# Kernel tuning notes

Measured on AMD Instinct MI355X. Metric: run time of the kernel, lower is better.

Reference implementation:

```python
import jax, jax.numpy as jnp
import numpy as np

P = 11  # corr_size (patch size of spatial_correlation_sample)
LEVELS = [(512, 64), (1024, 32), (512, 16), (256, 8), (256, 4), (256, 2)]  # (C, H) per pyramid level
B = 8


def _corr(f1, f2, p):
    # spatial_correlation_sample(kernel_size=1, patch_size=p, stride=1, padding=0, dilation_patch=1)
    # out[b, i*p+j, y, x] = sum_c f1[b,c,y,x] * f2[b,c,y+i-p//2, x+j-p//2] (zero padded)
    b, c, h, w = f1.shape
    r = p // 2
    f2p = jnp.pad(f2, ((0, 0), (0, 0), (r, r), (r, r)))
    shifts = jnp.stack(jnp.meshgrid(jnp.arange(p), jnp.arange(p), indexing='ij'), axis=-1).reshape(-1, 2)
    def body(carry, sh):
        sl = jax.lax.dynamic_slice(f2p, (0, 0, sh[0], sh[1]), (b, c, h, w))
        return carry, jnp.sum(f1 * sl, axis=1)  # (b, h, w)
    _, out = jax.lax.scan(body, None, shifts)  # (p*p, b, h, w)
    return jnp.transpose(out, (1, 0, 2, 3))  # (b, p*p, h, w)


def _cell(feat, feat_pre, h_pre, c_pre, W, bias, p):
    corr = _corr(feat, feat_pre, p)
    corr = jnp.where(corr > 0, corr, 0.01 * corr)  # LeakyReLU(0.01)
    corr = corr / jnp.max(corr)                    # max-normalize
    inp = jnp.concatenate([corr, h_pre], axis=1)   # (b, 2*p*p, h, w)
    conv = jax.lax.conv_general_dilated(
        inp, W, window_strides=(1, 1), padding=[(1, 1), (1, 1)],
        dimension_numbers=('NCHW', 'OIHW', 'NCHW')) + bias[None, :, None, None]
    cc_i, cc_f, cc_o, cc_g = jnp.split(conv, 4, axis=1)
    i = jax.nn.sigmoid(cc_i)
    f = jax.nn.sigmoid(cc_f)
    o = jax.nn.sigmoid(cc_o)
    g = jnp.tanh(cc_g)
    c_next = f * c_pre + i * g
    h_next = o * jnp.tanh(c_next)
    return h_next, c_next


def setup_inputs():
    key = jax.random.key(0)
    inp = {}
    for i, (C, H) in enumerate(LEVELS):
        ks = jax.random.split(jax.random.fold_in(key, i), 5)
        inp[f"x{i}"] = jax.random.normal(ks[0], (B, C, H, H), jnp.float32)
        inp[f"xp{i}"] = jax.random.normal(ks[1], (B, C, H, H), jnp.float32)
        inp[f"h{i}"] = jax.random.normal(ks[2], (B, P * P, H, H), jnp.float32)
        inp[f"c{i}"] = jax.random.normal(ks[3], (B, P * P, H, H), jnp.float32)
        inp[f"W{i}"] = jax.random.normal(ks[4], (4 * P * P, 2 * P * P, 3, 3), jnp.float32) * 0.02
        # bias: forget-gate slice initialized to 1 (as in init_weights)
        inp[f"bconv{i}"] = jnp.zeros((4 * P * P,), jnp.float32).at[P * P:2 * P * P].set(1.0)
    return inp


def reference(x0, x1, x2, x3, x4, x5, xp0, xp1, xp2, xp3, xp4, xp5,
              h0, h1, h2, h3, h4, h5, c0, c1, c2, c3, c4, c5,
              W0, W1, W2, W3, W4, W5, bconv0, bconv1, bconv2, bconv3, bconv4, bconv5):
    xs = [x0, x1, x2, x3, x4, x5]
    xps = [xp0, xp1, xp2, xp3, xp4, xp5]
    hs = [h0, h1, h2, h3, h4, h5]
    cs = [c0, c1, c2, c3, c4, c5]
    Ws = [W0, W1, W2, W3, W4, W5]
    bs = [bconv0, bconv1, bconv2, bconv3, bconv4, bconv5]
    outs = []
    for feat, fp, hp, cp, W, bias in zip(xs, xps, hs, cs, Ws, bs):
        hn, cn = _cell(feat, fp, hp, cp, W, bias, P)
        outs.extend([hn, cn])
    return tuple(outs)
```

## Files before the change

kernel.cpp:

```cpp
#include <hip/hip_runtime.h>
#include <hip/hip_bf16.h>
#include <cstdint>
#include <cstddef>

#define PD 11
#define PP 121
#define NB 8

typedef _Float16 f16x8 __attribute__((ext_vector_type(8)));
typedef float    f32x4 __attribute__((ext_vector_type(4)));

#define GLOAD16(SRC, DST) __builtin_amdgcn_global_load_lds( \
    (const __attribute__((address_space(1))) void*)(SRC),   \
    (__attribute__((address_space(3))) void*)(DST), 16, 0, 0)

struct TinyArgs {
    const float* x[3]; const float* xp[3]; const float* h[3];
    const float* c[3]; const float* w[3]; const float* bi[3];
    float* oh[3]; float* oc[3];
};

struct BigArgs {
    const float *x1, *xp1, *x2, *xp2;
    _Float16 *xT1, *xpT1, *xT2, *xpT2;
    _Float16 *inT0, *inT1, *inT2;
    const float *h0, *h1, *h2;
    const float *W0, *W1, *W2;
    _Float16 *ap0, *ap1, *ap2;
    unsigned* slots;
    const _Float16* zg;
};

struct ConvArgs {
    const _Float16 *inT0, *inT1, *inT2, *tinyInT;
    const float *c0, *c1, *c2;
    const _Float16 *ap0, *ap1, *ap2;
    const _Float16 *apT0, *apT1, *apT2;
    const float *bi0, *bi1, *bi2;
    float *oh0, *oc0, *oh1, *oc1, *oh2, *oc2;
    const _Float16* zg;
    TinyArgs ta;
};

__global__ void init_kernel(unsigned* __restrict__ slots, float* __restrict__ zg) {
    int t = threadIdx.x;
    if (t < 8) slots[t] = 0x007FFFFFu;
    for (int i = t; i < 1024; i += 256) zg[i] = 0.f;
}

__device__ __forceinline__ float decode_max(const unsigned* slot) {
    unsigned mu = *slot;
    return (mu & 0x80000000u) ? __uint_as_float(mu ^ 0x80000000u) : __uint_as_float(~mu);
}

template<int C, int H, int TPX>
__device__ void tpose_body(const float* __restrict__ in, _Float16* __restrict__ out,
                           int bx, int by, int tid, float (*s)[36])
{
    constexpr int W = H;
    const int b  = by / H, y = by % H;
    constexpr int NXT = W / TPX;
    const int x0 = (bx % NXT) * TPX;
    const int cc = (bx / NXT) * 64;

    constexpr int NF4 = 64 * TPX / 4;
    for (int f = tid; f < NF4; f += 256) {
        int r  = f / (TPX / 4);
        int xq = f % (TPX / 4);
        int col = (xq * 4) ^ (((r >> 3) & 7) * 4);
        *(float4*)&s[r][col] =
            *(const float4*)&in[((size_t)(b * C + cc + r) * H + y) * W + x0 + xq * 4];
    }
    __syncthreads();
    constexpr int NWT = TPX * 8;
    for (int t = tid; t < NWT; t += 256) {
        int pix = t >> 3, ck = t & 7;
        union { _Float16 h[8]; f16x8 v; } d;
#pragma unroll
        for (int j = 0; j < 8; ++j)
            d.h[j] = (_Float16)s[ck * 8 + j][pix ^ (ck * 4)];
        *(f16x8*)&out[((size_t)(b * H + y) * W + x0 + pix) * C + cc + ck * 8] = d.v;
    }
}

template<int C, int H, int TPX>
__global__ __launch_bounds__(256) void tpose_kernel(
    const float* __restrict__ xin, const float* __restrict__ xpin,
    _Float16* __restrict__ xT, _Float16* __restrict__ xpT)
{
    __shared__ float s[64][36];
    tpose_body<C, H, TPX>(blockIdx.z ? xpin : xin, blockIdx.z ? xpT : xT,
                          blockIdx.x, blockIdx.y, threadIdx.x, s);
}

template<int C, int H, int TSY, int TSX>
constexpr int corr_lds() {
    constexpr int HY = TSY + 10, HX = TSX + 10;
    constexpr int MZ = HY * HX;
    constexpr int MT = (MZ + 15) / 16;
    constexpr int MTP = MT * 16;
    constexpr int NPX = TSY * TSX;
    constexpr int BUF = (MTP + NPX) * 64;
    constexpr int ST2 = NPX + 8;
    constexpr int ST_B = MTP * ST2 * 2;
    return (2 * BUF > ST_B) ? 2 * BUF : ST_B;
}

template<int C, int H, int TSY, int TSX>
__device__ void corr_body(
    const _Float16* __restrict__ xT, const _Float16* __restrict__ xpT,
    const _Float16* __restrict__ zg,
    _Float16* __restrict__ inT, unsigned* __restrict__ slot,
    int bxt, int b, char* __restrict__ smem, float* __restrict__ sred)
{
    constexpr int W  = H;
    constexpr int HY = TSY + 10, HX = TSX + 10;
    constexpr int MZ = HY * HX;
    constexpr int MT = (MZ + 15) / 16;
    constexpr int MTP = MT * 16;
    constexpr int MFRAG = (MT + 7) / 8;
    constexpr int NPX = TSY * TSX;
    constexpr int NT  = NPX / 16;
    constexpr int KC  = C / 32;
    constexpr int ABYTES = MTP * 64;
    constexpr int BUF    = ABYTES + NPX * 64;
    constexpr int NLOAD  = BUF / 1024;
    constexpr int ST2    = NPX + 8;

    const int tid  = threadIdx.x;
    constexpr int TXT = W / TSX;
    const int y0 = (bxt / TXT) * TSY;
    const int x0 = (bxt % TXT) * TSX;
    const int w = tid >> 6, lane = tid & 63;
    const int lcol = lane & 15, lkg = lane >> 4;

    auto STAGE = [&](int bufsel, int kc) {
        char* dstb = smem + bufsel * BUF;
        int c = lane & 3;
        for (int it = w; it < NLOAD; it += 8) {
            const void* src;
            if (it < MTP / 16) {
                int z = it * 16 + (lane >> 2);
                int zy = y0 + z / HX - 5, zx = x0 + z % HX - 5;
                if (z < MZ && zy >= 0 && zy < H && zx >= 0 && zx < W)
                    src = xpT + ((size_t)(b * H + zy) * W + zx) * C + kc * 32 + ((c ^ (z >> 2)) & 3) * 8;
                else
                    src = zg + lane * 8;
            } else {
                int p = (it - MTP / 16) * 16 + (lane >> 2);
                int gy = y0 + p / TSX, gx = x0 + p % TSX;
                src = xT + ((size_t)(b * H + gy) * W + gx) * C + kc * 32 + ((c ^ (p >> 2)) & 3) * 8;
            }
            GLOAD16(src, dstb + it * 1024);
        }
    };

    f32x4 acc[MFRAG][NT];
#pragma unroll
    for (int i = 0; i < MFRAG; ++i)
#pragma unroll
        for (int nt = 0; nt < NT; ++nt)
            acc[i][nt] = (f32x4){0.f, 0.f, 0.f, 0.f};

    STAGE(0, 0);
    __syncthreads();
#pragma unroll 1
    for (int kc = 0; kc < KC; ++kc) {
        if (kc + 1 < KC) STAGE((kc + 1) & 1, kc + 1);
        const char* bb = smem + (kc & 1) * BUF;
        f16x8 bF[NT];
#pragma unroll
        for (int nt = 0; nt < NT; ++nt) {
            int p = nt * 16 + lcol;
            bF[nt] = *(const f16x8*)(bb + ABYTES + p * 64 + (((lkg ^ (p >> 2)) & 3) << 4));
        }
#pragma unroll
        for (int i = 0; i < MFRAG; ++i) {
            int mt = w + i * 8;
            if (mt < MT) {
                int z = mt * 16 + lcol;
                f16x8 aF = *(const f16x8*)(bb + z * 64 + (((lkg ^ (z >> 2)) & 3) << 4));
#pragma unroll
                for (int nt = 0; nt < NT; ++nt)
                    acc[i][nt] = __builtin_amdgcn_mfma_f32_16x16x32_f16(aF, bF[nt], acc[i][nt], 0, 0, 0);
            }
        }
        __syncthreads();
    }

    _Float16* sT = (_Float16*)smem;
#pragma unroll
    for (int i = 0; i < MFRAG; ++i) {
        int mt = w + i * 8;
        if (mt >= MT) continue;
        int z0 = mt * 16 + lkg * 4;
#pragma unroll
        for (int nt = 0; nt < NT; ++nt) {
            int p = nt * 16 + lcol;
#pragma unroll
            for (int r = 0; r < 4; ++r)
                sT[(z0 + r) * ST2 + p] = (_Float16)acc[i][nt][r];
        }
    }
    __syncthreads();

    float lmax = -3.4e38f;
    if (tid < NPX * 8) {
        int p  = tid >> 3;
        int qg = tid & 7;
        int py = p / TSX, px = p % TSX;
        size_t pix = (size_t)(b * H + y0 + py) * W + (x0 + px);
        unsigned* dst = (unsigned*)(inT + pix * 256) + qg * 8;
#pragma unroll
        for (int j2 = 0; j2 < 8; ++j2) {
            int q0 = qg * 16 + j2 * 2, q1 = q0 + 1;
            int qc0 = q0 < PP ? q0 : PP - 1;
            int qc1 = q1 < PP ? q1 : PP - 1;
            float v0 = (float)sT[((py + qc0 / PD) * HX + (px + qc0 % PD)) * ST2 + p];
            float v1 = (float)sT[((py + qc1 / PD) * HX + (px + qc1 % PD)) * ST2 + p];
            v0 = v0 > 0.f ? v0 : 0.01f * v0;
            v1 = v1 > 0.f ? v1 : 0.01f * v1;
            if (q0 < PP) lmax = fmaxf(lmax, v0);
            if (q1 < PP) lmax = fmaxf(lmax, v1);
            union { _Float16 h[2]; unsigned u; } pk;
            pk.h[0] = (_Float16)v0; pk.h[1] = (_Float16)v1;
            dst[j2] = pk.u;
        }
    }
    for (int off = 32; off; off >>= 1) lmax = fmaxf(lmax, __shfl_down(lmax, off));
    if (lane == 0) sred[w] = lmax;
    __syncthreads();
    if (tid == 0) {
        float m = sred[0];
        for (int i = 1; i < 8; ++i) m = fmaxf(m, sred[i]);
        unsigned eb = __float_as_uint(m);
        eb = (eb & 0x80000000u) ? ~eb : (eb | 0x80000000u);
        atomicMax(slot, eb);
    }
}

template<int C, int H, int TSY, int TSX>
__global__ __launch_bounds__(512, 2) void corr_mfma_kernel(
    const _Float16* __restrict__ xT, const _Float16* __restrict__ xpT,
    const _Float16* __restrict__ zg,
    _Float16* __restrict__ inT, unsigned* __restrict__ slot)
{
    __shared__ char smem[corr_lds<C, H, TSY, TSX>()];
    __shared__ float sred[8];
    corr_body<C, H, TSY, TSX>(xT, xpT, zg, inT, slot, blockIdx.x, blockIdx.y, smem, sred);
}

__device__ __forceinline__ void pack2_body(
    const float* __restrict__ Wsrc, _Float16* __restrict__ Apack,
    float inv, int mt, int ks, int tid, float* __restrict__ sW)
{
    const int icmax9 = (242 - ks * 32) * 9;
    for (int f = tid; f < 16 * 288; f += 256) {
        int r = f / 288, i = f - r * 288;
        int m = mt * 16 + r;
        float v = 0.f;
        if (m < 484 && i < icmax9) {
            int q = m >> 2, g = m & 3;
            v = Wsrc[((size_t)(g * PP + q) * 242 + ks * 32) * 9 + i];
        }
        sW[r * 292 + i] = v;
    }
    __syncthreads();
    const int o = tid * 2;
    const int l = o >> 3, e0 = o & 7;
    const int r = l & 15;
    const int klbase = (l >> 4) * 8;
    const int ic0 = ks * 32 + klbase + e0;
#pragma unroll 1
    for (int k9 = 0; k9 < 9; ++k9) {
        float v0 = sW[r * 292 + (klbase + e0) * 9 + k9];
        float v1 = sW[r * 292 + (klbase + e0 + 1) * 9 + k9];
        if (ic0 < PP)     v0 *= inv;
        if (ic0 + 1 < PP) v1 *= inv;
        union { _Float16 h[2]; unsigned u; } pk;
        pk.h[0] = (_Float16)v0; pk.h[1] = (_Float16)v1;
        *(unsigned*)((char*)Apack + (size_t)((k9 * 8 + ks) * 32 + mt) * 1024 + o * 2) = pk.u;
    }
}

template<int H>
__device__ void post_body(
    _Float16* __restrict__ inT, const float* __restrict__ hpre,
    const float* __restrict__ Wsrc, _Float16* __restrict__ Apack,
    const unsigned* __restrict__ slot, int bx, int tid, float* __restrict__ sW)
{
    if (bx < 256) {
        float inv = 1.0f / decode_max(slot);
        pack2_body(Wsrc, Apack, inv, bx >> 3, bx & 7, tid, sW);
        return;
    }
    constexpr int HW = H * H;
    constexpr int NP = NB * HW;
    int idx = (bx - 256) * 256 + tid;
    if (idx >= NP * 17) return;
    int c = 15 + idx / NP;
    int pix = idx % NP;
    int b = pix / HW, p2 = pix % HW;
    _Float16* base = inT + (size_t)pix * 256 + c * 8;
    union { _Float16 h[8]; uint4 u; } d;
    if (c == 15) {
        d.u = *(const uint4*)base;
#pragma unroll
        for (int j = 1; j < 8; ++j)
            d.h[j] = (_Float16)hpre[((size_t)b * PP + (j - 1)) * HW + p2];
    } else if (c <= 29) {
#pragma unroll
        for (int j = 0; j < 8; ++j)
            d.h[j] = (_Float16)hpre[((size_t)b * PP + (c * 8 + j - 121)) * HW + p2];
    } else if (c == 30) {
        d.h[0] = (_Float16)hpre[((size_t)b * PP + 119) * HW + p2];
        d.h[1] = (_Float16)hpre[((size_t)b * PP + 120) * HW + p2];
#pragma unroll
        for (int j = 2; j < 8; ++j) d.h[j] = (_Float16)0.f;
    } else {
#pragma unroll
        for (int j = 0; j < 8; ++j) d.h[j] = (_Float16)0.f;
    }
    *(uint4*)base = d.u;
}

template<int H>
__global__ __launch_bounds__(256) void post_kernel(
    _Float16* __restrict__ inT, const float* __restrict__ hpre,
    const float* __restrict__ Wsrc, _Float16* __restrict__ Apack,
    const unsigned* __restrict__ slot)
{
    __shared__ float sW[16 * 292];
    post_body<H>(inT, hpre, Wsrc, Apack, slot, blockIdx.x, threadIdx.x, sW);
}

template<int H>
__device__ void corr_small512_body(const float* __restrict__ x, const float* __restrict__ xp,
    _Float16* __restrict__ inT, unsigned* __restrict__ slot, int b, int bx,
    float* __restrict__ sred)
{
    constexpr int PX  = H * H;
    constexpr int TOT = PX * PP;
    const int tid = threadIdx.x;
    const int o = bx * 512 + tid;
    float v = -3.4e38f;
    if (o < TOT) {
        int p = o / PP;
        int q = o - p * PP;
        int y = p / H, xx = p % H;
        int sy = y + q / PD - 5, sx = xx + q % PD - 5;
        float acc = 0.f;
        if (sy >= 0 && sy < H && sx >= 0 && sx < H) {
            const float* xb  = x  + (size_t)b * 256 * PX + p;
            const float* xpb = xp + (size_t)b * 256 * PX + sy * H + sx;
#pragma unroll 8
            for (int c = 0; c < 256; ++c)
                acc = fmaf(xb[c * PX], xpb[c * PX], acc);
        }
        float lv = acc > 0.f ? acc : 0.01f * acc;
        inT[((size_t)b * PX + p) * 256 + q] = (_Float16)lv;
        v = lv;
    }
    for (int off = 32; off; off >>= 1) v = fmaxf(v, __shfl_down(v, off));
    if ((tid & 63) == 0) sred[tid >> 6] = v;
    __syncthreads();
    if (tid == 0) {
        float m = sred[0];
        for (int i = 1; i < 8; ++i) m = fmaxf(m, sred[i]);
        unsigned eb = __float_as_uint(m);
        eb = (eb & 0x80000000u) ? ~eb : (eb | 0x80000000u);
        atomicMax(slot, eb);
    }
}

template<int H>
__device__ void hfill_body(_Float16* __restrict__ inT, const float* __restrict__ hpre,
                           int b, int bx)
{
    constexpr int HW = H * H;
    int idx = bx * 256 + threadIdx.x;
    if (idx >= HW * 17) return;
    int c = 15 + idx / HW;
    int p2 = idx % HW;
    _Float16* base = inT + ((size_t)b * HW + p2) * 256 + c * 8;
    union { _Float16 h[8]; uint4 u; } d;
    if (c == 15) {
        d.u = *(const uint4*)base;
#pragma unroll
        for (int j = 1; j < 8; ++j)
            d.h[j] = (_Float16)hpre[((size_t)b * PP + (j - 1)) * HW + p2];
    } else if (c <= 29) {
#pragma unroll
        for (int j = 0; j < 8; ++j)
            d.h[j] = (_Float16)hpre[((size_t)b * PP + (c * 8 + j - 121)) * HW + p2];
    } else if (c == 30) {
        d.h[0] = (_Float16)hpre[((size_t)b * PP + 119) * HW + p2];
        d.h[1] = (_Float16)hpre[((size_t)b * PP + 120) * HW + p2];
#pragma unroll
        for (int j = 2; j < 8; ++j) d.h[j] = (_Float16)0.f;
    } else {
#pragma unroll
        for (int j = 0; j < 8; ++j) d.h[j] = (_Float16)0.f;
    }
    *(uint4*)base = d.u;
}

__global__ __launch_bounds__(256) void mixA_kernel(BigArgs ba, _Float16* __restrict__ inT0)
{
    __shared__ float sW[16 * 292];
    const int i = blockIdx.x, tid = threadIdx.x;
    if (i < 2432) {
        post_body<64>(inT0, ba.h0, ba.W0, ba.ap0, ba.slots + 0, i, tid, sW);
    } else if (i < 2432 + 8192) {
        int j = i - 2432;
        int z = j >> 12, r = j & 4095;
        tpose_body<1024, 32, 32>(z ? ba.xp1 : ba.x1, z ? ba.xpT1 : ba.xT1,
                                 r & 15, r >> 4, tid, (float(*)[36])sW);
    } else {
        int j = i - (2432 + 8192);
        int z = j >> 10, r = j & 1023;
        tpose_body<512, 16, 16>(z ? ba.xp2 : ba.x2, z ? ba.xpT2 : ba.xT2,
                                r & 7, r >> 3, tid, (float(*)[36])sW);
    }
}

__global__ __launch_bounds__(512, 2) void mixB_kernel(BigArgs ba, TinyArgs ta,
                                                      _Float16* __restrict__ tinyInT)
{
    __shared__ char smem[36864];
    __shared__ float sred[8];
    const int i = blockIdx.x;
    if (i < 256) {
        corr_body<1024, 32, 4, 8>(ba.xT1, ba.xpT1, ba.zg, ba.inT1, ba.slots + 1,
                                  i & 31, i >> 5, smem, sred);
    } else if (i < 384) {
        int j = i - 256;
        corr_body<512, 16, 4, 4>(ba.xT2, ba.xpT2, ba.zg, ba.inT2, ba.slots + 2,
                                 j & 15, j >> 4, smem, sred);
    } else if (i < 512) {
        int j = i - 384;
        corr_small512_body<8>(ta.x[0], ta.xp[0], tinyInT, ba.slots + 3,
                              j >> 4, j & 15, sred);
    } else if (i < 544) {
        int j = i - 512;
        corr_small512_body<4>(ta.x[1], ta.xp[1], tinyInT + 131072, ba.slots + 4,
                              j >> 2, j & 3, sred);
    } else {
        int j = i - 544;
        corr_small512_body<2>(ta.x[2], ta.xp[2], tinyInT + 163840, ba.slots + 5,
                              j, 0, sred);
    }
}

__global__ __launch_bounds__(256) void mixC_kernel(BigArgs ba, TinyArgs ta,
    _Float16* __restrict__ tinyInT,
    _Float16* __restrict__ apT0, _Float16* __restrict__ apT1, _Float16* __restrict__ apT2)
{
    __shared__ float sW[16 * 292];
    const int i = blockIdx.x, tid = threadIdx.x;
    if (i < 800) {
        post_body<32>(ba.inT1, ba.h1, ba.W1, ba.ap1, ba.slots + 1, i, tid, sW);
    } else if (i < 1192) {
        post_body<16>(ba.inT2, ba.h2, ba.W2, ba.ap2, ba.slots + 2, i - 800, tid, sW);
    } else if (i < 1960) {
        int j = i - 1192;
        int z = j >> 8, bx = j & 255;
        _Float16* Ap = (z == 0) ? apT0 : (z == 1 ? apT1 : apT2);
        float inv = 1.0f / decode_max(ba.slots + 3 + z);
        pack2_body(ta.w[z], Ap, inv, bx >> 3, bx & 7, tid, sW);
    } else {
        int j = i - 1960;
        if (j < 40)      hfill_body<8>(tinyInT,          ta.h[0], j / 5, j % 5);
        else if (j < 56) { int k = j - 40; hfill_body<4>(tinyInT + 131072, ta.h[1], k / 2, k % 2); }
        else             hfill_body<2>(tinyInT + 163840, ta.h[2], j - 56, 0);
    }
}

template<int H, int TR, int MSPLIT>
__device__ void conv_mfma3_body(
    const _Float16* __restrict__ inT, const float* __restrict__ cpre,
    const _Float16* __restrict__ Apack, const float* __restrict__ bias,
    const _Float16* __restrict__ zg,
    float* __restrict__ outh, float* __restrict__ outc,
    int tile, int b, int mblk, char* __restrict__ sB)
{
    constexpr int W = H;
    constexpr int TC = 16, SR = TC + 2;
    constexpr int NPOS = (TR + 2) * SR;
    constexpr int MT_BLK = 32 / MSPLIT;
    constexpr int AF = 4 / MSPLIT;
    constexpr int TILES_X = W / TC;

    const int tid  = threadIdx.x;
    const int ty0  = (tile / TILES_X) * TR;
    const int tx0  = (tile % TILES_X) * TC;
    const int w = tid >> 6, lane = tid & 63;
    const int lcol = lane & 15, kg = lane >> 4;

    for (int it = w; it < NPOS / 2; it += 8) {
        int r  = it * 2 + (lane >> 5);
        int c  = lane & 31;
        int iy = r / SR, ix = r % SR;
        int gy = ty0 + iy - 1, gx = tx0 + ix - 1;
        const void* src;
        if (gy >= 0 && gy < H && gx >= 0 && gx < W)
            src = inT + ((size_t)(b * H + gy) * W + gx) * 256 + (c ^ (ix & 7)) * 8;
        else
            src = zg + lane * 8;
        GLOAD16(src, sB + it * 1024);
    }
    __syncthreads();

    const int mtg0 = mblk * MT_BLK + w * AF;

    f32x4 acc[AF * TR];
#pragma unroll
    for (int a = 0; a < AF; ++a) {
        int q = (mtg0 + a) * 4 + kg;
        f32x4 bv;
#pragma unroll
        for (int r = 0; r < 4; ++r) bv[r] = (q < PP) ? bias[r * PP + q] : 0.f;
#pragma unroll
        for (int j = 0; j < TR; ++j) acc[a * TR + j] = bv;
    }

    const f16x8* apL = (const f16x8*)Apack + (size_t)mtg0 * 64 + lane;

    auto COMPUTE = [&](const f16x8* af, int s) {
        int k9 = s >> 3, ks = s & 7;
        int ky = k9 / 3, kx = k9 - ky * 3;
        int ix = lcol + kx;
        int xsw = (ix & 7) << 4;
        int cb  = kg * 16 + ks * 64;
        __builtin_amdgcn_s_setprio(1);
#pragma unroll
        for (int j = 0; j < TR; ++j) {
            int addr = ((((j + ky) * SR + ix) * 512) + cb) ^ xsw;
            f16x8 bf = *(const f16x8*)(sB + addr);
#pragma unroll
            for (int a = 0; a < AF; ++a)
                acc[a * TR + j] = __builtin_amdgcn_mfma_f32_16x16x32_f16(af[a], bf, acc[a * TR + j], 0, 0, 0);
        }
        __builtin_amdgcn_s_setprio(0);
    };

    f16x8 afA[AF], afB[AF];
#pragma unroll
    for (int a = 0; a < AF; ++a) afA[a] = apL[a * 64];
#pragma unroll 1
    for (int s2 = 0; s2 < 36; ++s2) {
        const f16x8* apB = apL + (size_t)(s2 * 2 + 1) * 2048;
#pragma unroll
        for (int a = 0; a < AF; ++a) afB[a] = apB[a * 64];
        COMPUTE(afA, s2 * 2);
        if (s2 < 35) {
            const f16x8* apA = apL + (size_t)(s2 * 2 + 2) * 2048;
#pragma unroll
            for (int a = 0; a < AF; ++a) afA[a] = apA[a * 64];
        }
        COMPUTE(afB, s2 * 2 + 1);
    }

#pragma unroll
    for (int a = 0; a < AF; ++a) {
        int q = (mtg0 + a) * 4 + kg;
        if (q >= PP) continue;
#pragma unroll
        for (int j = 0; j < TR; ++j) {
            int y = ty0 + j, x = tx0 + lcol;
            if (y >= H) continue;
            float ai = acc[a * TR + j][0];
            float af_ = acc[a * TR + j][1];
            float ao = acc[a * TR + j][2];
            float ag = acc[a * TR + j][3];
            float ig = 1.f / (1.f + expf(-ai));
            float fg = 1.f / (1.f + expf(-af_));
            float og = 1.f / (1.f + expf(-ao));
            float gg = tanhf(ag);
            size_t oidx = (((size_t)b * PP + q) * H + y) * W + x;
            float cp = cpre[oidx];
            float cn = fg * cp + ig * gg;
            outh[oidx] = og * tanhf(cn);
            outc[oidx] = cn;
        }
    }
}

template<int H>
__device__ void conv_tiny_body(const _Float16* __restrict__ inT,
    const float* __restrict__ cpre, const _Float16* __restrict__ Apack,
    const float* __restrict__ bias, float* __restrict__ outh,
    float* __restrict__ outc, int b, int mblk, char* __restrict__ sB)
{
    constexpr int NPX = H * H;
    constexpr int NT  = (NPX + 15) / 16;
    constexpr int SR  = H + 2;
    constexpr int NPOS = SR * SR;
    const int tid = threadIdx.x;

    constexpr int CHUNKS = NPOS * 32;
    for (int flat = tid; flat < CHUNKS; flat += 512) {
        int cg  = flat & 31;
        int pos = flat >> 5;
        int iy = pos / SR, ix = pos % SR;
        int gy = iy - 1, gx = ix - 1;
        f16x8 v = {0, 0, 0, 0, 0, 0, 0, 0};
        if (gy >= 0 && gy < H && gx >= 0 && gx < H)
            v = *(const f16x8*)(inT + ((size_t)(b * H + gy) * H + gx) * 256 + cg * 8);
        int dst = (pos * 512 + cg * 16) ^ ((ix & 7) << 4);
        *(f16x8*)(sB + dst) = v;
    }
    __syncthreads();

    const int w = tid >> 6, lane = tid & 63;
    const int lcol = lane & 15, kg = lane >> 4;
    const int mt = mblk * 8 + w;
    const int q  = mt * 4 + kg;

    f32x4 acc[NT];
    f32x4 bv;
#pragma unroll
    for (int r = 0; r < 4; ++r) bv[r] = (q < PP) ? bias[r * PP + q] : 0.f;
#pragma unroll
    for (int nt = 0; nt < NT; ++nt) acc[nt] = bv;

#pragma unroll 1
    for (int k9 = 0; k9 < 9; ++k9) {
        const int ky = k9 / 3, kx = k9 % 3;
        int basev[NT], xswv[NT];
#pragma unroll
        for (int nt = 0; nt < NT; ++nt) {
            int p = nt * 16 + lcol;
            int pc = (NPX < 16 && p >= NPX) ? 0 : p;
            int py = pc / H, px = pc % H;
            int iy = py + ky, ix = px + kx;
            basev[nt] = (iy * SR + ix) * 512 + kg * 16;
            xswv[nt]  = (ix & 7) << 4;
        }
        const f16x8* apb = (const f16x8*)Apack + ((size_t)(k9 * 8) * 32 + mt) * 64 + lane;
#pragma unroll 1
        for (int ks = 0; ks < 8; ++ks) {
            f16x8 bf[NT];
#pragma unroll
            for (int nt = 0; nt < NT; ++nt) {
                bf[nt] = *(const f16x8*)(sB + ((basev[nt] + ks * 64) ^ xswv[nt]));
                if (NPX < 16 && nt * 16 + lcol >= NPX) bf[nt] = (f16x8){};
            }
            f16x8 af = apb[(size_t)ks * 32 * 64];
#pragma unroll
            for (int nt = 0; nt < NT; ++nt)
                acc[nt] = __builtin_amdgcn_mfma_f32_16x16x32_f16(af, bf[nt], acc[nt], 0, 0, 0);
        }
    }

    if (q < PP) {
#pragma unroll
        for (int nt = 0; nt < NT; ++nt) {
            int p = nt * 16 + lcol;
            if (NPX < 16 && p >= NPX) continue;
            int py = p / H, px = p % H;
            float ai = acc[nt][0];
            float af_ = acc[nt][1];
            float ao = acc[nt][2];
            float ag = acc[nt][3];
            float ig = 1.f / (1.f + expf(-ai));
            float fg = 1.f / (1.f + expf(-af_));
            float og = 1.f / (1.f + expf(-ao));
            float gg = tanhf(ag);
            size_t oidx = (((size_t)b * PP + q) * H + py) * H + px;
            float cp = cpre[oidx];
            float cn = fg * cp + ig * gg;
            outh[oidx] = og * tanhf(cn);
            outc[oidx] = cn;
        }
    }
}

__global__ __launch_bounds__(512, 4) void conv_combo_kernel(ConvArgs ca)
{
    __shared__ char sB[108 * 512];
    const int bx = blockIdx.x;
    if (bx < 512) {
        conv_mfma3_body<64, 4, 1>(ca.inT0, ca.c0, ca.ap0, ca.bi0, ca.zg,
                                  ca.oh0, ca.oc0, bx & 63, bx >> 6, 0, sB);
    } else if (bx < 768) {
        int i = bx - 512;
        conv_mfma3_body<32, 4, 2>(ca.inT1, ca.c1, ca.ap1, ca.bi1, ca.zg,
                                  ca.oh1, ca.oc1, i & 15, (i >> 4) & 7, i >> 7, sB);
    } else if (bx < 896) {
        int i = bx - 768;
        conv_mfma3_body<16, 4, 4>(ca.inT2, ca.c2, ca.ap2, ca.bi2, ca.zg,
                                  ca.oh2, ca.oc2, i & 3, (i >> 2) & 7, i >> 5, sB);
    } else {
        int j = bx - 896;
        int z = j >> 5, r = j & 31;
        int b = r >> 2, mblk = r & 3;
        if      (z == 0) conv_tiny_body<8>(ca.tinyInT,          ca.ta.c[0], ca.apT0, ca.ta.bi[0], ca.ta.oh[0], ca.ta.oc[0], b, mblk, sB);
        else if (z == 1) conv_tiny_body<4>(ca.tinyInT + 131072, ca.ta.c[1], ca.apT1, ca.ta.bi[1], ca.ta.oh[1], ca.ta.oc[1], b, mblk, sB);
        else             conv_tiny_body<2>(ca.tinyInT + 163840, ca.ta.c[2], ca.apT2, ca.ta.bi[2], ca.ta.oh[2], ca.ta.oc[2], b, mblk, sB);
    }
}

extern "C" void kernel_launch(void* const* d_in, const int* in_sizes, int n_in,
                              void* d_out, int out_size, void* d_ws, size_t ws_size,
                              hipStream_t stream) {
    (void)in_sizes; (void)n_in; (void)out_size; (void)ws_size;
    static const int HH[6] = {64, 32, 16, 8, 4, 2};

    char* W = (char*)d_ws;
    unsigned* maxslots = (unsigned*)W;
    _Float16* Apack0 = (_Float16*)(W + 256);
    _Float16* inT0   = (_Float16*)(W + 2359808);
    char* XB = W + 19137024;
    char* PB = W + 52691456;
    _Float16* xT0  = (_Float16*)XB;
    _Float16* xpT0 = (_Float16*)PB;
    _Float16* zg   = (_Float16*)(W + 86245888);

    BigArgs ba;
    ba.x1  = (const float*)d_in[6];  ba.xp1 = (const float*)d_in[7];
    ba.x2  = (const float*)d_in[12]; ba.xp2 = (const float*)d_in[13];
    ba.xT1  = (_Float16*)(XB + 0);
    ba.xpT1 = (_Float16*)(XB + 16777216);
    ba.xT2  = (_Float16*)(PB + 0);
    ba.xpT2 = (_Float16*)(PB + 2097152);
    ba.inT0 = inT0;
    ba.inT1 = (_Float16*)(PB + 4194304);
    ba.inT2 = (_Float16*)(PB + 8388608);
    ba.h0 = (const float*)d_in[2];  ba.h1 = (const float*)d_in[8];  ba.h2 = (const float*)d_in[14];
    ba.W0 = (const float*)d_in[4];  ba.W1 = (const float*)d_in[10]; ba.W2 = (const float*)d_in[16];
    ba.ap0 = Apack0;
    ba.ap1 = (_Float16*)(PB + 9437184);
    ba.ap2 = (_Float16*)(PB + 11796480);
    ba.slots = maxslots;
    ba.zg = zg;
    _Float16* tinyInT = (_Float16*)(PB + 16777216);
    _Float16* apT0 = (_Float16*)(PB + 17825792);
    _Float16* apT1 = (_Float16*)(PB + 20185088);
    _Float16* apT2 = (_Float16*)(PB + 22544384);

    float* out = (float*)d_out;
    size_t obase[6];
    {
        size_t ob = 0;
        for (int L = 0; L < 6; ++L) { obase[L] = ob; ob += 2ull * NB * PP * HH[L] * HH[L]; }
    }

    TinyArgs ta;
    for (int i = 0; i < 3; ++i) {
        int L = 3 + i;
        ta.x[i]  = (const float*)d_in[6 * L + 0];
        ta.xp[i] = (const float*)d_in[6 * L + 1];
        ta.h[i]  = (const float*)d_in[6 * L + 2];
        ta.c[i]  = (const float*)d_in[6 * L + 3];
        ta.w[i]  = (const float*)d_in[6 * L + 4];
        ta.bi[i] = (const float*)d_in[6 * L + 5];
        int S = NB * PP * HH[L] * HH[L];
        ta.oh[i] = out + obase[L];
        ta.oc[i] = out + obase[L] + S;
    }

    init_kernel<<<1, 256, 0, stream>>>(maxslots, (float*)zg);
    tpose_kernel<512, 64, 32><<<dim3(16, NB * 64, 2), 256, 0, stream>>>(
        (const float*)d_in[0], (const float*)d_in[1], xT0, xpT0);
    corr_mfma_kernel<512, 64, 8, 8><<<dim3(64, NB), 512, 0, stream>>>(
        xT0, xpT0, zg, inT0, maxslots + 0);
    mixA_kernel<<<2432 + 8192 + 2048, 256, 0, stream>>>(ba, inT0);
    mixB_kernel<<<552, 512, 0, stream>>>(ba, ta, tinyInT);
    mixC_kernel<<<2024, 256, 0, stream>>>(ba, ta, tinyInT, apT0, apT1, apT2);
    ConvArgs ca;
    ca.inT0 = inT0; ca.inT1 = ba.inT1; ca.inT2 = ba.inT2; ca.tinyInT = tinyInT;
    ca.c0 = (const float*)d_in[3];  ca.c1 = (const float*)d_in[9];  ca.c2 = (const float*)d_in[15];
    ca.ap0 = Apack0; ca.ap1 = ba.ap1; ca.ap2 = ba.ap2;
    ca.apT0 = apT0; ca.apT1 = apT1; ca.apT2 = apT2;
    ca.bi0 = (const float*)d_in[5]; ca.bi1 = (const float*)d_in[11]; ca.bi2 = (const float*)d_in[17];
    ca.oh0 = out + obase[0]; ca.oc0 = out + obase[0] + NB * PP * 64 * 64;
    ca.oh1 = out + obase[1]; ca.oc1 = out + obase[1] + NB * PP * 32 * 32;
    ca.oh2 = out + obase[2]; ca.oc2 = out + obase[2] + NB * PP * 16 * 16;
    ca.zg = zg;
    ca.ta = ta;
    conv_combo_kernel<<<896 + 96, 512, 0, stream>>>(ca);
}
```

Measured before the change: 268.5 us.

## Regroup pre-conv kernels to overlap tiny-level work with big-level stages

Reorganizes the launch schedule: the level-0 transpose now shares a launch with the tiny-level correlations, the level-0 correlation shares one with the tiny h-fill, and the level-1/2 transposes are merged with level-0 post processing and tiny weight packing. Helper bodies now use blockDim strides and guard threads above 256 so they can run inside 512-thread blocks. The aim is to fill idle CUs during the big stages and cut the number of serial launch boundaries. The tiny input buffer moves to its own workspace region so it no longer aliases buffers in use at the same time. In exchange, the transpose and pack blocks now run at 512 threads with half of them idle in some phases.

```diff
diff --git a/kernel.cpp b/kernel.cpp
--- a/kernel.cpp
+++ b/kernel.cpp
@@ -62,9 +62,10 @@
     constexpr int NXT = W / TPX;
     const int x0 = (bx % NXT) * TPX;
     const int cc = (bx / NXT) * 64;
+    const int stride = blockDim.x;
 
     constexpr int NF4 = 64 * TPX / 4;
-    for (int f = tid; f < NF4; f += 256) {
+    for (int f = tid; f < NF4; f += stride) {
         int r  = f / (TPX / 4);
         int xq = f % (TPX / 4);
         int col = (xq * 4) ^ (((r >> 3) & 7) * 4);
@@ -73,7 +74,7 @@
     }
     __syncthreads();
     constexpr int NWT = TPX * 8;
-    for (int t = tid; t < NWT; t += 256) {
+    for (int t = tid; t < NWT; t += stride) {
         int pix = t >> 3, ck = t & 7;
         union { _Float16 h[8]; f16x8 v; } d;
 #pragma unroll
@@ -81,29 +82,6 @@
             d.h[j] = (_Float16)s[ck * 8 + j][pix ^ (ck * 4)];
         *(f16x8*)&out[((size_t)(b * H + y) * W + x0 + pix) * C + cc + ck * 8] = d.v;
     }
-}
-
-template<int C, int H, int TPX>
-__global__ __launch_bounds__(256) void tpose_kernel(
-    const float* __restrict__ xin, const float* __restrict__ xpin,
-    _Float16* __restrict__ xT, _Float16* __restrict__ xpT)
-{
-    __shared__ float s[64][36];
-    tpose_body<C, H, TPX>(blockIdx.z ? xpin : xin, blockIdx.z ? xpT : xT,
-                          blockIdx.x, blockIdx.y, threadIdx.x, s);
-}
-
-template<int C, int H, int TSY, int TSX>
-constexpr int corr_lds() {
-    constexpr int HY = TSY + 10, HX = TSX + 10;
-    constexpr int MZ = HY * HX;
-    constexpr int MT = (MZ + 15) / 16;
-    constexpr int MTP = MT * 16;
-    constexpr int NPX = TSY * TSX;
-    constexpr int BUF = (MTP + NPX) * 64;
-    constexpr int ST2 = NPX + 8;
-    constexpr int ST_B = MTP * ST2 * 2;
-    return (2 * BUF > ST_B) ? 2 * BUF : ST_B;
 }
 
 template<int C, int H, int TSY, int TSX>
@@ -239,23 +217,13 @@
     }
 }
 
-template<int C, int H, int TSY, int TSX>
-__global__ __launch_bounds__(512, 2) void corr_mfma_kernel(
-    const _Float16* __restrict__ xT, const _Float16* __restrict__ xpT,
-    const _Float16* __restrict__ zg,
-    _Float16* __restrict__ inT, unsigned* __restrict__ slot)
-{
-    __shared__ char smem[corr_lds<C, H, TSY, TSX>()];
-    __shared__ float sred[8];
-    corr_body<C, H, TSY, TSX>(xT, xpT, zg, inT, slot, blockIdx.x, blockIdx.y, smem, sred);
-}
-
 __device__ __forceinline__ void pack2_body(
     const float* __restrict__ Wsrc, _Float16* __restrict__ Apack,
     float inv, int mt, int ks, int tid, float* __restrict__ sW)
 {
     const int icmax9 = (242 - ks * 32) * 9;
-    for (int f = tid; f < 16 * 288; f += 256) {
+    const int stride = blockDim.x;
+    for (int f = tid; f < 16 * 288; f += stride) {
         int r = f / 288, i = f - r * 288;
         int m = mt * 16 + r;
         float v = 0.f;
@@ -266,20 +234,22 @@
         sW[r * 292 + i] = v;
     }
     __syncthreads();
-    const int o = tid * 2;
-    const int l = o >> 3, e0 = o & 7;
-    const int r = l & 15;
-    const int klbase = (l >> 4) * 8;
-    const int ic0 = ks * 32 + klbase + e0;
+    if (tid < 256) {
+        const int o = tid * 2;
+        const int l = o >> 3, e0 = o & 7;
+        const int r = l & 15;
+        const int klbase = (l >> 4) * 8;
+        const int ic0 = ks * 32 + klbase + e0;
 #pragma unroll 1
-    for (int k9 = 0; k9 < 9; ++k9) {
-        float v0 = sW[r * 292 + (klbase + e0) * 9 + k9];
-        float v1 = sW[r * 292 + (klbase + e0 + 1) * 9 + k9];
-        if (ic0 < PP)     v0 *= inv;
-        if (ic0 + 1 < PP) v1 *= inv;
-        union { _Float16 h[2]; unsigned u; } pk;
-        pk.h[0] = (_Float16)v0; pk.h[1] = (_Float16)v1;
-        *(unsigned*)((char*)Apack + (size_t)((k9 * 8 + ks) * 32 + mt) * 1024 + o * 2) = pk.u;
+        for (int k9 = 0; k9 < 9; ++k9) {
+            float v0 = sW[r * 292 + (klbase + e0) * 9 + k9];
+            float v1 = sW[r * 292 + (klbase + e0 + 1) * 9 + k9];
+            if (ic0 < PP)     v0 *= inv;
+            if (ic0 + 1 < PP) v1 *= inv;
+            union { _Float16 h[2]; unsigned u; } pk;
+            pk.h[0] = (_Float16)v0; pk.h[1] = (_Float16)v1;
+            *(unsigned*)((char*)Apack + (size_t)((k9 * 8 + ks) * 32 + mt) * 1024 + o * 2) = pk.u;
+        }
     }
 }
 
@@ -294,6 +264,7 @@
         pack2_body(Wsrc, Apack, inv, bx >> 3, bx & 7, tid, sW);
         return;
     }
+    if (tid >= 256) return;
     constexpr int HW = H * H;
     constexpr int NP = NB * HW;
     int idx = (bx - 256) * 256 + tid;
@@ -322,16 +293,6 @@
         for (int j = 0; j < 8; ++j) d.h[j] = (_Float16)0.f;
     }
     *(uint4*)base = d.u;
-}
-
-template<int H>
-__global__ __launch_bounds__(256) void post_kernel(
-    _Float16* __restrict__ inT, const float* __restrict__ hpre,
-    const float* __restrict__ Wsrc, _Float16* __restrict__ Apack,
-    const unsigned* __restrict__ slot)
-{
-    __shared__ float sW[16 * 292];
-    post_body<H>(inT, hpre, Wsrc, Apack, slot, blockIdx.x, threadIdx.x, sW);
 }
 
 template<int H>
@@ -377,6 +338,7 @@
 __device__ void hfill_body(_Float16* __restrict__ inT, const float* __restrict__ hpre,
                            int b, int bx)
 {
+    if (threadIdx.x >= 256) return;
     constexpr int HW = H * H;
     int idx = bx * 256 + threadIdx.x;
     if (idx >= HW * 17) return;
@@ -405,27 +367,69 @@
     *(uint4*)base = d.u;
 }
 
-__global__ __launch_bounds__(256) void mixA_kernel(BigArgs ba, _Float16* __restrict__ inT0)
+__global__ __launch_bounds__(512, 2) void mixPre_kernel(
+    const float* __restrict__ x0, const float* __restrict__ xp0,
+    _Float16* __restrict__ xT0, _Float16* __restrict__ xpT0,
+    TinyArgs ta, _Float16* __restrict__ tinyInT, unsigned* __restrict__ slots)
+{
+    __shared__ float s[64][36];
+    __shared__ float sred[8];
+    const int bx = blockIdx.x;
+    if (bx < 16384) {
+        int z = bx >> 13, r = bx & 8191;
+        tpose_body<512, 64, 32>(z ? xp0 : x0, z ? xpT0 : xT0, r & 15, r >> 4, threadIdx.x, s);
+    } else {
+        int j = bx - 16384;
+        if (j < 128)      corr_small512_body<8>(ta.x[0], ta.xp[0], tinyInT,          slots + 3, j >> 4, j & 15, sred);
+        else if (j < 160) { int k = j - 128; corr_small512_body<4>(ta.x[1], ta.xp[1], tinyInT + 131072, slots + 4, k >> 2, k & 3, sred); }
+        else              corr_small512_body<2>(ta.x[2], ta.xp[2], tinyInT + 163840, slots + 5, j - 160, 0, sred);
+    }
+}
+
+__global__ __launch_bounds__(512, 2) void mix0_kernel(
+    const _Float16* __restrict__ xT0, const _Float16* __restrict__ xpT0,
+    const _Float16* __restrict__ zg, _Float16* __restrict__ inT0,
+    unsigned* __restrict__ slots, TinyArgs ta, _Float16* __restrict__ tinyInT)
+{
+    __shared__ char smem[51200];
+    __shared__ float sred[8];
+    const int bx = blockIdx.x;
+    if (bx < 512) {
+        corr_body<512, 64, 8, 8>(xT0, xpT0, zg, inT0, slots + 0, bx & 63, bx >> 6, smem, sred);
+    } else {
+        int j = bx - 512;
+        if (j < 40)      hfill_body<8>(tinyInT,          ta.h[0], j / 5, j % 5);
+        else if (j < 56) { int k = j - 40; hfill_body<4>(tinyInT + 131072, ta.h[1], k >> 1, k & 1); }
+        else             hfill_body<2>(tinyInT + 163840, ta.h[2], j - 56, 0);
+    }
+}
+
+__global__ __launch_bounds__(512) void mixD_kernel(BigArgs ba, TinyArgs ta,
+    _Float16* __restrict__ inT0,
+    _Float16* __restrict__ apT0, _Float16* __restrict__ apT1, _Float16* __restrict__ apT2)
 {
     __shared__ float sW[16 * 292];
-    const int i = blockIdx.x, tid = threadIdx.x;
-    if (i < 2432) {
-        post_body<64>(inT0, ba.h0, ba.W0, ba.ap0, ba.slots + 0, i, tid, sW);
-    } else if (i < 2432 + 8192) {
-        int j = i - 2432;
+    const int j = blockIdx.x;
+    const int tid = threadIdx.x;
+    if (j < 8192) {
         int z = j >> 12, r = j & 4095;
         tpose_body<1024, 32, 32>(z ? ba.xp1 : ba.x1, z ? ba.xpT1 : ba.xT1,
                                  r & 15, r >> 4, tid, (float(*)[36])sW);
-    } else {
-        int j = i - (2432 + 8192);
-        int z = j >> 10, r = j & 1023;
+    } else if (j < 10240) {
+        int k = j - 8192, z = k >> 10, r = k & 1023;
         tpose_body<512, 16, 16>(z ? ba.xp2 : ba.x2, z ? ba.xpT2 : ba.xT2,
                                 r & 7, r >> 3, tid, (float(*)[36])sW);
-    }
-}
-
-__global__ __launch_bounds__(512, 2) void mixB_kernel(BigArgs ba, TinyArgs ta,
-                                                      _Float16* __restrict__ tinyInT)
+    } else if (j < 12672) {
+        post_body<64>(inT0, ba.h0, ba.W0, ba.ap0, ba.slots + 0, j - 10240, tid, sW);
+    } else {
+        int k = j - 12672, z = k >> 8, bxp = k & 255;
+        _Float16* Ap = (z == 0) ? apT0 : (z == 1 ? apT1 : apT2);
+        float inv = 1.0f / decode_max(ba.slots + 3 + z);
+        pack2_body(ta.w[z], Ap, inv, bxp >> 3, bxp & 7, tid, sW);
+    }
+}
+
+__global__ __launch_bounds__(512, 2) void mixE_kernel(BigArgs ba)
 {
     __shared__ char smem[36864];
     __shared__ float sred[8];
@@ -433,47 +437,19 @@
     if (i < 256) {
         corr_body<1024, 32, 4, 8>(ba.xT1, ba.xpT1, ba.zg, ba.inT1, ba.slots + 1,
                                   i & 31, i >> 5, smem, sred);
-    } else if (i < 384) {
+    } else {
         int j = i - 256;
         corr_body<512, 16, 4, 4>(ba.xT2, ba.xpT2, ba.zg, ba.inT2, ba.slots + 2,
                                  j & 15, j >> 4, smem, sred);
-    } else if (i < 512) {
-        int j = i - 384;
-        corr_small512_body<8>(ta.x[0], ta.xp[0], tinyInT, ba.slots + 3,
-                              j >> 4, j & 15, sred);
-    } else if (i < 544) {
-        int j = i - 512;
-        corr_small512_body<4>(ta.x[1], ta.xp[1], tinyInT + 131072, ba.slots + 4,
-                              j >> 2, j & 3, sred);
-    } else {
-        int j = i - 544;
-        corr_small512_body<2>(ta.x[2], ta.xp[2], tinyInT + 163840, ba.slots + 5,
-                              j, 0, sred);
-    }
-}
-
-__global__ __launch_bounds__(256) void mixC_kernel(BigArgs ba, TinyArgs ta,
-    _Float16* __restrict__ tinyInT,
-    _Float16* __restrict__ apT0, _Float16* __restrict__ apT1, _Float16* __restrict__ apT2)
+    }
+}
+
+__global__ __launch_bounds__(256) void mixF_kernel(BigArgs ba)
 {
     __shared__ float sW[16 * 292];
-    const int i = blockIdx.x, tid = threadIdx.x;
-    if (i < 800) {
-        post_body<32>(ba.inT1, ba.h1, ba.W1, ba.ap1, ba.slots + 1, i, tid, sW);
-    } else if (i < 1192) {
-        post_body<16>(ba.inT2, ba.h2, ba.W2, ba.ap2, ba.slots + 2, i - 800, tid, sW);
-    } else if (i < 1960) {
-        int j = i - 1192;
-        int z = j >> 8, bx = j & 255;
-        _Float16* Ap = (z == 0) ? apT0 : (z == 1 ? apT1 : apT2);
-        float inv = 1.0f / decode_max(ba.slots + 3 + z);
-        pack2_body(ta.w[z], Ap, inv, bx >> 3, bx & 7, tid, sW);
-    } else {
-        int j = i - 1960;
-        if (j < 40)      hfill_body<8>(tinyInT,          ta.h[0], j / 5, j % 5);
-        else if (j < 56) { int k = j - 40; hfill_body<4>(tinyInT + 131072, ta.h[1], k / 2, k % 2); }
-        else             hfill_body<2>(tinyInT + 163840, ta.h[2], j - 56, 0);
-    }
+    const int i = blockIdx.x;
+    if (i < 800) post_body<32>(ba.inT1, ba.h1, ba.W1, ba.ap1, ba.slots + 1, i, threadIdx.x, sW);
+    else         post_body<16>(ba.inT2, ba.h2, ba.W2, ba.ap2, ba.slots + 2, i - 800, threadIdx.x, sW);
 }
 
 template<int H, int TR, int MSPLIT>
@@ -716,6 +692,7 @@
     _Float16* xT0  = (_Float16*)XB;
     _Float16* xpT0 = (_Float16*)PB;
     _Float16* zg   = (_Float16*)(W + 86245888);
+    _Float16* tinyInT = (_Float16*)(W + 86249984);
 
     BigArgs ba;
     ba.x1  = (const float*)d_in[6];  ba.xp1 = (const float*)d_in[7];
@@ -734,7 +711,6 @@
     ba.ap2 = (_Float16*)(PB + 11796480);
     ba.slots = maxslots;
     ba.zg = zg;
-    _Float16* tinyInT = (_Float16*)(PB + 16777216);
     _Float16* apT0 = (_Float16*)(PB + 17825792);
     _Float16* apT1 = (_Float16*)(PB + 20185088);
     _Float16* apT2 = (_Float16*)(PB + 22544384);
@@ -761,13 +737,12 @@
     }
 
     init_kernel<<<1, 256, 0, stream>>>(maxslots, (float*)zg);
-    tpose_kernel<512, 64, 32><<<dim3(16, NB * 64, 2), 256, 0, stream>>>(
-        (const float*)d_in[0], (const float*)d_in[1], xT0, xpT0);
-    corr_mfma_kernel<512, 64, 8, 8><<<dim3(64, NB), 512, 0, stream>>>(
-        xT0, xpT0, zg, inT0, maxslots + 0);
-    mixA_kernel<<<2432 + 8192 + 2048, 256, 0, stream>>>(ba, inT0);
-    mixB_kernel<<<552, 512, 0, stream>>>(ba, ta, tinyInT);
-    mixC_kernel<<<2024, 256, 0, stream>>>(ba, ta, tinyInT, apT0, apT1, apT2);
+    mixPre_kernel<<<16384 + 168, 512, 0, stream>>>(
+        (const float*)d_in[0], (const float*)d_in[1], xT0, xpT0, ta, tinyInT, maxslots);
+    mix0_kernel<<<512 + 64, 512, 0, stream>>>(xT0, xpT0, zg, inT0, maxslots, ta, tinyInT);
+    mixD_kernel<<<8192 + 2048 + 2432 + 768, 512, 0, stream>>>(ba, ta, inT0, apT0, apT1, apT2);
+    mixE_kernel<<<384, 512, 0, stream>>>(ba);
+    mixF_kernel<<<1192, 256, 0, stream>>>(ba);
     ConvArgs ca;
     ca.inT0 = inT0; ca.inT1 = ba.inT1; ca.inT2 = ba.inT2; ca.tinyInT = tinyInT;
     ca.c0 = (const float*)d_in[3];  ca.c1 = (const float*)d_in[9];  ca.c2 = (const float*)d_in[15];
```

Result: slower. 285.0 us (+6.2%).
